# Kernel tuning notes

Measured on AMD Instinct MI355X. Metric: run time of the kernel, lower is better.

Reference implementation:

```python
import jax, jax.numpy as jnp
import numpy as np

FEATURE_DIM = 256
KEEP = 64  # low-frequency block size kept after the pseudo-DCT


def setup_inputs() -> dict:
    key = jax.random.key(0)
    k_x, k_w, k_b = jax.random.split(key, 3)
    B, C, H, W = 32, 3, 512, 512
    x = jax.random.uniform(k_x, (B, C, H, W), dtype=jnp.float32)
    # nn.Linear(64*64, feature_dim): weight [out, in], bias [out]
    fan_in = KEEP * KEEP
    bound = 1.0 / np.sqrt(fan_in)
    fc_w = jax.random.uniform(k_w, (FEATURE_DIM, fan_in), dtype=jnp.float32, minval=-bound, maxval=bound)
    fc_b = jax.random.uniform(k_b, (FEATURE_DIM,), dtype=jnp.float32, minval=-bound, maxval=bound)
    return {"x": x, "fc_w": fc_w, "fc_b": fc_b}


def reference(x, fc_w, fc_b):
    # grayscale conversion (input has 3 channels)
    x_gray = 0.299 * x[:, 0] + 0.587 * x[:, 1] + 0.114 * x[:, 2]  # [B, H, W]
    # "dct2d": FFT along last dim, then FFT along second-to-last, real part
    X = jnp.fft.fft(jnp.fft.fft(x_gray, axis=-1), axis=-2).real  # [B, H, W]
    # keep low-frequency 64x64 block and flatten
    coeffs = X[:, :KEEP, :KEEP].reshape(x.shape[0], KEEP * KEEP)  # [B, 4096]
    # final linear projection
    return coeffs @ fc_w.T + fc_b  # [B, feature_dim]
```

## Files before the change

### kernel.cpp

```cpp
#include <hip/hip_runtime.h>
#include <hip/hip_bf16.h>

#define HW_ (512 * 512)

typedef __attribute__((ext_vector_type(8))) _Float16 half8;
typedef __attribute__((ext_vector_type(4))) _Float16 half4;
typedef __attribute__((ext_vector_type(4))) float    f32x4;

__global__ __launch_bounds__(256) void k_prep(_Float16* __restrict__ basisA) {
    int i = blockIdx.x * 256 + threadIdx.x;
    if (i < 128 * 512) {
        int r = i >> 9, h = i & 511;
        int ph = ((r & 63) * h) & 511;
        float ang = (float)ph * (6.28318530717958647692f / 512.0f);
        basisA[i] = (_Float16)((r < 64) ? cosf(ang) : sinf(ang));
    }
}

__global__ __launch_bounds__(256) void k1(const float* __restrict__ x,
                                          const _Float16* __restrict__ basisA,
                                          _Float16* __restrict__ P)
{
    __shared__ _Float16 g[32][520];
    int h0 = blockIdx.x * 32;
    int b  = blockIdx.y;
    int t  = threadIdx.x;
    const float* xb = x + (size_t)b * 3 * HW_;

    for (int i = 0; i < 16; ++i) {
        int slot = t + i * 256;
        int hh = slot >> 7;
        int w4 = slot & 127;
        const float* p = xb + (size_t)(h0 + hh) * 512 + w4 * 4;
        float4 r  = *(const float4*)p;
        float4 gg = *(const float4*)(p + HW_);
        float4 bb = *(const float4*)(p + 2 * HW_);
        half4 o;
        o.x = (_Float16)(0.299f * r.x + 0.587f * gg.x + 0.114f * bb.x);
        o.y = (_Float16)(0.299f * r.y + 0.587f * gg.y + 0.114f * bb.y);
        o.z = (_Float16)(0.299f * r.z + 0.587f * gg.z + 0.114f * bb.z);
        o.w = (_Float16)(0.299f * r.w + 0.587f * gg.w + 0.114f * bb.w);
        *(half4*)&g[hh][w4 * 4] = o;
    }
    __syncthreads();

    int lane = t & 63, wv = t >> 6, l15 = lane & 15, quad = lane >> 4;
    f32x4 acc[2][2];
    for (int i = 0; i < 2; ++i)
        for (int j = 0; j < 2; ++j) acc[i][j] = (f32x4){0.f, 0.f, 0.f, 0.f};

    for (int k0 = 0; k0 < 512; k0 += 32) {
        int kc = k0 + quad * 8;
        half8 a[2], bv[2];
        for (int mi = 0; mi < 2; ++mi)
            a[mi] = *(const half8*)(basisA + (wv * 32 + mi * 16 + l15) * 512 + kc);
        for (int ni = 0; ni < 2; ++ni)
            bv[ni] = *(const half8*)&g[ni * 16 + l15][kc];
        for (int mi = 0; mi < 2; ++mi)
            for (int ni = 0; ni < 2; ++ni)
                acc[mi][ni] = __builtin_amdgcn_mfma_f32_16x16x32_f16(
                    a[mi], bv[ni], acc[mi][ni], 0, 0, 0);
    }

    _Float16* Pb = P + (size_t)b * 128 * 512;
    for (int mi = 0; mi < 2; ++mi)
        for (int ni = 0; ni < 2; ++ni)
            for (int r = 0; r < 4; ++r) {
                int m = wv * 32 + mi * 16 + quad * 4 + r;
                int h = h0 + ni * 16 + l15;
                float v = acc[mi][ni][r];
                if (m >= 64) v = -v;
                Pb[m * 512 + h] = (_Float16)v;
            }
}

__global__ __launch_bounds__(128) void k2(const _Float16* __restrict__ basisA,
                                          const _Float16* __restrict__ P,
                                          _Float16* __restrict__ X)
{
    int b     = blockIdx.y;
    int mbase = blockIdx.x * 32 + (threadIdx.x >> 6) * 16;
    int lane  = threadIdx.x & 63, l15 = lane & 15, quad = lane >> 4;

    f32x4 acc[4];
    for (int i = 0; i < 4; ++i) acc[i] = (f32x4){0.f, 0.f, 0.f, 0.f};

    const _Float16* Pb = P + (size_t)b * 128 * 512;

    for (int k0 = 0; k0 < 1024; k0 += 32) {
        int kc  = k0 + quad * 8;
        int hi  = (kc >= 512) ? 64 : 0;
        int col = kc & 511;
        half8 a = *(const half8*)(basisA + (hi + mbase + l15) * 512 + col);
        for (int ni = 0; ni < 4; ++ni) {
            half8 bv = *(const half8*)(Pb + (hi + ni * 16 + l15) * 512 + col);
            acc[ni] = __builtin_amdgcn_mfma_f32_16x16x32_f16(a, bv, acc[ni], 0, 0, 0);
        }
    }

    _Float16* Xb = X + (size_t)b * 4096;
    for (int ni = 0; ni < 4; ++ni)
        for (int r = 0; r < 4; ++r) {
            int kh = mbase + quad * 4 + r;
            int kw = ni * 16 + l15;
            Xb[kh * 64 + kw] = (_Float16)(acc[ni][r] * 0.0625f);
        }
}

__global__ __launch_bounds__(64) void k3(const _Float16* __restrict__ X,
                                         const float* __restrict__ fc_w,
                                         const float* __restrict__ fc_b,
                                         float* __restrict__ out)
{
    int nb  = blockIdx.x & 15;
    int kcb = blockIdx.x >> 4;
    int lane = threadIdx.x, l15 = lane & 15, quad = lane >> 4;

    f32x4 acc[2];
    acc[0] = (f32x4){0.f, 0.f, 0.f, 0.f};
    acc[1] = (f32x4){0.f, 0.f, 0.f, 0.f};

    int kbeg = kcb * 1024;
    for (int k0 = kbeg; k0 < kbeg + 1024; k0 += 32) {
        int kk = k0 + quad * 8;
        half8 a0 = *(const half8*)(X + (size_t)l15 * 4096 + kk);
        half8 a1 = *(const half8*)(X + (size_t)(16 + l15) * 4096 + kk);
        const float* wp = fc_w + (size_t)(nb * 16 + l15) * 4096 + kk;
        float4 f0 = *(const float4*)wp;
        float4 f1 = *(const float4*)(wp + 4);
        half8 b0;
        b0[0] = (_Float16)(f0.x * 16.0f);
        b0[1] = (_Float16)(f0.y * 16.0f);
        b0[2] = (_Float16)(f0.z * 16.0f);
        b0[3] = (_Float16)(f0.w * 16.0f);
        b0[4] = (_Float16)(f1.x * 16.0f);
        b0[5] = (_Float16)(f1.y * 16.0f);
        b0[6] = (_Float16)(f1.z * 16.0f);
        b0[7] = (_Float16)(f1.w * 16.0f);
        acc[0] = __builtin_amdgcn_mfma_f32_16x16x32_f16(a0, b0, acc[0], 0, 0, 0);
        acc[1] = __builtin_amdgcn_mfma_f32_16x16x32_f16(a1, b0, acc[1], 0, 0, 0);
    }

    for (int mi = 0; mi < 2; ++mi)
        for (int r = 0; r < 4; ++r) {
            int m = mi * 16 + quad * 4 + r;
            int f = nb * 16 + l15;
            float v = acc[mi][r];
            if (kcb == 0) v += fc_b[f];
            atomicAdd(out + m * 256 + f, v);
        }
}

extern "C" void kernel_launch(void* const* d_in, const int* in_sizes, int n_in,
                              void* d_out, int out_size, void* d_ws, size_t ws_size,
                              hipStream_t stream) {
    const float* x    = (const float*)d_in[0];
    const float* fc_w = (const float*)d_in[1];
    const float* fc_b = (const float*)d_in[2];
    float* out = (float*)d_out;

    char* ws = (char*)d_ws;
    _Float16* basisA = (_Float16*)(ws + 0);
    _Float16* P      = (_Float16*)(ws + 131072);
    _Float16* X      = (_Float16*)(ws + 4325376);

    k_prep<<<256, 256, 0, stream>>>(basisA);
    k1<<<dim3(16, 32), 256, 0, stream>>>(x, basisA, P);
    k2<<<dim3(2, 32), 128, 0, stream>>>(basisA, P, X);
    hipMemsetAsync(d_out, 0, (size_t)out_size * sizeof(float), stream);
    k3<<<64, 64, 0, stream>>>(X, fc_w, fc_b, out);
}
```

Measured before the change: 188.8 us.

## Compute DFT basis on the fly, fuse grayscale loads, drop atomics and memset

Removes the basis-precompute kernel and generates cos/sin twiddles inline with fast intrinsics inside both DFT GEMM kernels. The grayscale conversion is fused into the k1 MFMA loop, reading x directly from global memory instead of staging it in LDS. The final projection kernel reduces its K-split partials in shared memory and writes the output directly, eliminating the memset and the atomics. This trades launch and memory traffic for extra transcendental VALU work and redundant global loads of x.

```diff
diff --git a/kernel.cpp b/kernel.cpp
--- a/kernel.cpp
+++ b/kernel.cpp
@@ -2,60 +2,62 @@
 #include <hip/hip_bf16.h>
 
 #define HW_ (512 * 512)
+#define STEP_ (6.28318530717958647692f / 512.0f)
 
 typedef __attribute__((ext_vector_type(8))) _Float16 half8;
-typedef __attribute__((ext_vector_type(4))) _Float16 half4;
 typedef __attribute__((ext_vector_type(4))) float    f32x4;
 
-__global__ __launch_bounds__(256) void k_prep(_Float16* __restrict__ basisA) {
-    int i = blockIdx.x * 256 + threadIdx.x;
-    if (i < 128 * 512) {
-        int r = i >> 9, h = i & 511;
-        int ph = ((r & 63) * h) & 511;
-        float ang = (float)ph * (6.28318530717958647692f / 512.0f);
-        basisA[i] = (_Float16)((r < 64) ? cosf(ang) : sinf(ang));
-    }
-}
-
 __global__ __launch_bounds__(256) void k1(const float* __restrict__ x,
-                                          const _Float16* __restrict__ basisA,
                                           _Float16* __restrict__ P)
 {
-    __shared__ _Float16 g[32][520];
     int h0 = blockIdx.x * 32;
     int b  = blockIdx.y;
     int t  = threadIdx.x;
+    int lane = t & 63, wv = t >> 6, l15 = lane & 15, quad = lane >> 4;
     const float* xb = x + (size_t)b * 3 * HW_;
 
-    for (int i = 0; i < 16; ++i) {
-        int slot = t + i * 256;
-        int hh = slot >> 7;
-        int w4 = slot & 127;
-        const float* p = xb + (size_t)(h0 + hh) * 512 + w4 * 4;
-        float4 r  = *(const float4*)p;
-        float4 gg = *(const float4*)(p + HW_);
-        float4 bb = *(const float4*)(p + 2 * HW_);
-        half4 o;
-        o.x = (_Float16)(0.299f * r.x + 0.587f * gg.x + 0.114f * bb.x);
-        o.y = (_Float16)(0.299f * r.y + 0.587f * gg.y + 0.114f * bb.y);
-        o.z = (_Float16)(0.299f * r.z + 0.587f * gg.z + 0.114f * bb.z);
-        o.w = (_Float16)(0.299f * r.w + 0.587f * gg.w + 0.114f * bb.w);
-        *(half4*)&g[hh][w4 * 4] = o;
-    }
-    __syncthreads();
-
-    int lane = t & 63, wv = t >> 6, l15 = lane & 15, quad = lane >> 4;
     f32x4 acc[2][2];
     for (int i = 0; i < 2; ++i)
         for (int j = 0; j < 2; ++j) acc[i][j] = (f32x4){0.f, 0.f, 0.f, 0.f};
 
+    int  r6[2];
+    bool issin[2];
+    for (int mi = 0; mi < 2; ++mi) {
+        int row = wv * 32 + mi * 16 + l15;
+        r6[mi]    = row & 63;
+        issin[mi] = row >= 64;
+    }
+
     for (int k0 = 0; k0 < 512; k0 += 32) {
         int kc = k0 + quad * 8;
-        half8 a[2], bv[2];
+
+        half8 a[2];
         for (int mi = 0; mi < 2; ++mi)
-            a[mi] = *(const half8*)(basisA + (wv * 32 + mi * 16 + l15) * 512 + kc);
-        for (int ni = 0; ni < 2; ++ni)
-            bv[ni] = *(const half8*)&g[ni * 16 + l15][kc];
+            for (int j = 0; j < 8; ++j) {
+                int ph = (r6[mi] * (kc + j)) & 511;
+                float ang = (float)ph * STEP_;
+                a[mi][j] = (_Float16)(issin[mi] ? __sinf(ang) : __cosf(ang));
+            }
+
+        half8 bv[2];
+        for (int ni = 0; ni < 2; ++ni) {
+            const float* p = xb + (size_t)(h0 + ni * 16 + l15) * 512 + kc;
+            float4 r0 = *(const float4*)p;
+            float4 r1 = *(const float4*)(p + 4);
+            float4 g0 = *(const float4*)(p + HW_);
+            float4 g1 = *(const float4*)(p + HW_ + 4);
+            float4 b0 = *(const float4*)(p + 2 * HW_);
+            float4 b1 = *(const float4*)(p + 2 * HW_ + 4);
+            bv[ni][0] = (_Float16)(0.299f * r0.x + 0.587f * g0.x + 0.114f * b0.x);
+            bv[ni][1] = (_Float16)(0.299f * r0.y + 0.587f * g0.y + 0.114f * b0.y);
+            bv[ni][2] = (_Float16)(0.299f * r0.z + 0.587f * g0.z + 0.114f * b0.z);
+            bv[ni][3] = (_Float16)(0.299f * r0.w + 0.587f * g0.w + 0.114f * b0.w);
+            bv[ni][4] = (_Float16)(0.299f * r1.x + 0.587f * g1.x + 0.114f * b1.x);
+            bv[ni][5] = (_Float16)(0.299f * r1.y + 0.587f * g1.y + 0.114f * b1.y);
+            bv[ni][6] = (_Float16)(0.299f * r1.z + 0.587f * g1.z + 0.114f * b1.z);
+            bv[ni][7] = (_Float16)(0.299f * r1.w + 0.587f * g1.w + 0.114f * b1.w);
+        }
+
         for (int mi = 0; mi < 2; ++mi)
             for (int ni = 0; ni < 2; ++ni)
                 acc[mi][ni] = __builtin_amdgcn_mfma_f32_16x16x32_f16(
@@ -74,8 +76,7 @@
             }
 }
 
-__global__ __launch_bounds__(128) void k2(const _Float16* __restrict__ basisA,
-                                          const _Float16* __restrict__ P,
+__global__ __launch_bounds__(128) void k2(const _Float16* __restrict__ P,
                                           _Float16* __restrict__ X)
 {
     int b     = blockIdx.y;
@@ -86,14 +87,22 @@
     for (int i = 0; i < 4; ++i) acc[i] = (f32x4){0.f, 0.f, 0.f, 0.f};
 
     const _Float16* Pb = P + (size_t)b * 128 * 512;
+    int rm = mbase + l15;
 
     for (int k0 = 0; k0 < 1024; k0 += 32) {
-        int kc  = k0 + quad * 8;
-        int hi  = (kc >= 512) ? 64 : 0;
-        int col = kc & 511;
-        half8 a = *(const half8*)(basisA + (hi + mbase + l15) * 512 + col);
+        int kc   = k0 + quad * 8;
+        bool iss = kc >= 512;
+        int col  = kc & 511;
+        int hi   = iss ? 64 : 0;
+
+        half8 a;
+        for (int j = 0; j < 8; ++j) {
+            int ph = (rm * (col + j)) & 511;
+            float ang = (float)ph * STEP_;
+            a[j] = (_Float16)(iss ? __sinf(ang) : __cosf(ang));
+        }
         for (int ni = 0; ni < 4; ++ni) {
-            half8 bv = *(const half8*)(Pb + (hi + ni * 16 + l15) * 512 + col);
+            half8 bv = *(const half8*)(Pb + (size_t)(hi + ni * 16 + l15) * 512 + col);
             acc[ni] = __builtin_amdgcn_mfma_f32_16x16x32_f16(a, bv, acc[ni], 0, 0, 0);
         }
     }
@@ -107,20 +116,21 @@
         }
 }
 
-__global__ __launch_bounds__(64) void k3(const _Float16* __restrict__ X,
-                                         const float* __restrict__ fc_w,
-                                         const float* __restrict__ fc_b,
-                                         float* __restrict__ out)
+__global__ __launch_bounds__(256) void k3(const _Float16* __restrict__ X,
+                                          const float* __restrict__ fc_w,
+                                          const float* __restrict__ fc_b,
+                                          float* __restrict__ out)
 {
-    int nb  = blockIdx.x & 15;
-    int kcb = blockIdx.x >> 4;
-    int lane = threadIdx.x, l15 = lane & 15, quad = lane >> 4;
+    __shared__ float part[4][32][16];
+    int nb = blockIdx.x;
+    int t  = threadIdx.x;
+    int lane = t & 63, wv = t >> 6, l15 = lane & 15, quad = lane >> 4;
 
     f32x4 acc[2];
     acc[0] = (f32x4){0.f, 0.f, 0.f, 0.f};
     acc[1] = (f32x4){0.f, 0.f, 0.f, 0.f};
 
-    int kbeg = kcb * 1024;
+    int kbeg = wv * 1024;
     for (int k0 = kbeg; k0 < kbeg + 1024; k0 += 32) {
         int kk = k0 + quad * 8;
         half8 a0 = *(const half8*)(X + (size_t)l15 * 4096 + kk);
@@ -142,13 +152,17 @@
     }
 
     for (int mi = 0; mi < 2; ++mi)
-        for (int r = 0; r < 4; ++r) {
-            int m = mi * 16 + quad * 4 + r;
-            int f = nb * 16 + l15;
-            float v = acc[mi][r];
-            if (kcb == 0) v += fc_b[f];
-            atomicAdd(out + m * 256 + f, v);
-        }
+        for (int r = 0; r < 4; ++r)
+            part[wv][mi * 16 + quad * 4 + r][l15] = acc[mi][r];
+    __syncthreads();
+
+    for (int e = 0; e < 2; ++e) {
+        int o = t + e * 256;
+        int m = o >> 4, fi = o & 15;
+        float v = part[0][m][fi] + part[1][m][fi] + part[2][m][fi] + part[3][m][fi]
+                + fc_b[nb * 16 + fi];
+        out[m * 256 + nb * 16 + fi] = v;
+    }
 }
 
 extern "C" void kernel_launch(void* const* d_in, const int* in_sizes, int n_in,
@@ -160,13 +174,10 @@
     float* out = (float*)d_out;
 
     char* ws = (char*)d_ws;
-    _Float16* basisA = (_Float16*)(ws + 0);
-    _Float16* P      = (_Float16*)(ws + 131072);
-    _Float16* X      = (_Float16*)(ws + 4325376);
+    _Float16* P = (_Float16*)(ws + 0);
+    _Float16* X = (_Float16*)(ws + 4194304);
 
-    k_prep<<<256, 256, 0, stream>>>(basisA);
-    k1<<<dim3(16, 32), 256, 0, stream>>>(x, basisA, P);
-    k2<<<dim3(2, 32), 128, 0, stream>>>(basisA, P, X);
-    hipMemsetAsync(d_out, 0, (size_t)out_size * sizeof(float), stream);
-    k3<<<64, 64, 0, stream>>>(X, fc_w, fc_b, out);
+    k1<<<dim3(16, 32), 256, 0, stream>>>(x, P);
+    k2<<<dim3(2, 32), 128, 0, stream>>>(P, X);
+    k3<<<16, 256, 0, stream>>>(X, fc_w, fc_b, out);
 }
```

New measurement: 196.7 us. 4.2% more time.
